# Kernel tuning notes

Hardware: AMD Instinct MI355X
Metric: run time of the kernel (lower is better)

## Reference

```python
import jax, jax.numpy as jnp
import numpy as np


def _segsum(x):
    """Stable segment sum: exp(segsum(A)) is 1-semiseparable. x: (..., T) -> (..., T, T)."""
    T = x.shape[-1]
    xx = jnp.broadcast_to(x[..., None], (*x.shape, T))
    xx = jnp.where(jnp.tril(jnp.ones((T, T), bool), -1), xx, 0.0)
    s = jnp.cumsum(xx, axis=-2)
    return jnp.where(jnp.tril(jnp.ones((T, T), bool), 0), s, -jnp.inf)


def setup_inputs() -> dict:
    key = jax.random.key(0)
    ks = jax.random.split(key, 6)
    b, T, h, p, n = 2, 1024, 32, 64, 128
    x = jax.random.normal(ks[0], (b, T, h, p), jnp.float32)
    # negative decay rates, as produced by -exp(A_log)*softplus(dt) in Mamba2
    A = -jax.random.uniform(ks[1], (b, T, h), jnp.float32, minval=0.01, maxval=0.5)
    B = jax.random.normal(ks[2], (b, T, h, n), jnp.float32)
    C = jax.random.normal(ks[3], (b, T, h, n), jnp.float32)
    # retrieval similarity mask (lower-triangular, like segment_and_cosine_similarity output)
    L_mask = jax.random.uniform(ks[4], (b, h, T, T), jnp.float32) * jnp.tril(jnp.ones((T, T), jnp.float32))
    mask_scaling_factor = jnp.float32(0.5)
    return {"x": x, "A": A, "B": B, "C": C, "L_mask": L_mask,
            "mask_scaling_factor": mask_scaling_factor, "chunk_size": 64}


def reference(x, A, B, C, L_mask, mask_scaling_factor, chunk_size):
    b, T, h, p = x.shape
    n = B.shape[-1]
    l = chunk_size
    k = T // l
    # chunk: b (c l) ... -> b c l ...
    xr = x.reshape(b, k, l, h, p)
    Br = B.reshape(b, k, l, h, n)
    Cr = C.reshape(b, k, l, h, n)
    Ar = jnp.transpose(A.reshape(b, k, l, h), (0, 3, 1, 2))  # b h c l
    A_cs = jnp.cumsum(Ar, axis=-1)                            # b h c l
    L = jnp.exp(_segsum(Ar))                                  # b h c l l
    # decompose_diagonal_and_lower_tri(L_mask, chunk_size)
    r = L_mask.reshape(b, h, k, l, k, l)
    didx = np.arange(k)
    L_mask_diag = jnp.moveaxis(r[:, :, didx, :, didx, :], 0, 2)          # b h k l l
    row_idx, col_idx = np.tril_indices(k, -1)                             # strict lower block pairs
    lower_tri = jnp.moveaxis(r[:, :, row_idx, :, col_idx, :], 0, 2)       # b h P l l
    L = L + mask_scaling_factor * L_mask_diag
    # diagonal (intra-chunk) blocks
    Y_diag = jnp.einsum('bclhn,bcshn,bhcls,bcshp->bclhp', Cr, Br, L, xr)
    # retrieval off-diagonal blocks, scatter-added back per destination chunk
    Y_tmp = jnp.einsum('bclhn,bcshn,bhcls,bcshp->bclhp',
                       Cr[:, row_idx], Br[:, col_idx],
                       mask_scaling_factor * lower_tri, xr[:, col_idx])   # b P l h p
    Y_retr = jnp.moveaxis(
        jax.ops.segment_sum(jnp.moveaxis(Y_tmp, 1, 0), jnp.asarray(row_idx), num_segments=k),
        0, 1)                                                             # b k l h p
    # inter-chunk state passing
    decay_states = jnp.exp(A_cs[..., -1:] - A_cs)                         # b h c l
    states = jnp.einsum('bclhn,bhcl,bclhp->bchpn', Br, decay_states, xr)  # b c h p n
    states = jnp.concatenate([jnp.zeros_like(states[:, :1]), states], axis=1)
    decay_chunk = jnp.exp(_segsum(jnp.pad(A_cs[..., -1], ((0, 0), (0, 0), (1, 0)))))  # b h (k+1) (k+1)
    new_states = jnp.einsum('bhzc,bchpn->bzhpn', decay_chunk, states)
    states_in, final_state = new_states[:, :-1], new_states[:, -1]
    Y_off = jnp.einsum('bclhn,bchpn,bhcl->bclhp', Cr, states_in, jnp.exp(A_cs))
    Y = (Y_diag + Y_off + Y_retr).reshape(b, T, h, p)
    return Y, final_state
```

## Files before the change

kernel.cpp:

```cpp
#include <hip/hip_runtime.h>

#define T_ 1024
#define H_ 32
#define P_ 64
#define N_ 128
#define L_ 64

typedef float f32x4 __attribute__((ext_vector_type(4)));
typedef short short8 __attribute__((ext_vector_type(8)));
typedef short short4v __attribute__((ext_vector_type(4)));
typedef unsigned int uint2v __attribute__((ext_vector_type(2)));
typedef unsigned int uint4v __attribute__((ext_vector_type(4)));

#define LOG2E 1.4426950408889634f

static __device__ __forceinline__ float bf2f(short s) {
  return __uint_as_float(((unsigned int)(unsigned short)s) << 16);
}

static __device__ __forceinline__ unsigned cvt_pk_bf16(float lo, float hi) {
  unsigned r;
  asm("v_cvt_pk_bf16_f32 %0, %1, %2" : "=v"(r) : "v"(lo), "v"(hi));
  return r;
}

static __device__ __forceinline__ float fexp2(float x) {
#if __has_builtin(__builtin_amdgcn_exp2f)
  return __builtin_amdgcn_exp2f(x);
#else
  return __expf(x * 0.6931471805599453f);
#endif
}

__global__ __launch_bounds__(256) void prep_kernel(
    const float* __restrict__ x, const float* __restrict__ Bm,
    const float* __restrict__ Cm, const float* __restrict__ A,
    short* __restrict__ Bbf, short* __restrict__ BT,
    short* __restrict__ Cbf, short* __restrict__ xT,
    float* __restrict__ cumA) {
  const int bh = blockIdx.x;
  const int tb = blockIdx.y;
  const int b = bh >> 5, h = bh & 31;
  const int tid = threadIdx.x;

  if (tb == 16) {
    __shared__ float sc[256];
    const int t0 = 4 * tid;
    const float a0 = A[(size_t)(b * T_ + t0 + 0) * H_ + h];
    const float a1 = A[(size_t)(b * T_ + t0 + 1) * H_ + h];
    const float a2 = A[(size_t)(b * T_ + t0 + 2) * H_ + h];
    const float a3 = A[(size_t)(b * T_ + t0 + 3) * H_ + h];
    const float p1 = a0 + a1, p2 = p1 + a2, p3 = p2 + a3;
    sc[tid] = p3;
    __syncthreads();
    for (int off = 1; off < 256; off <<= 1) {
      float v = (tid >= off) ? sc[tid - off] : 0.0f;
      __syncthreads();
      sc[tid] += v;
      __syncthreads();
    }
    const float base = sc[tid] - p3;
    float4 o;
    o.x = (base + a0) * LOG2E;
    o.y = (base + p1) * LOG2E;
    o.z = (base + p2) * LOG2E;
    o.w = (base + p3) * LOG2E;
    *(float4*)(cumA + (size_t)bh * T_ + t0) = o;
    return;
  }

  __shared__ short Bt[128][72];
  __shared__ short Xt[64][72];

#pragma unroll
  for (int i = 0; i < 8; ++i) {
    const int idx = tid + 256 * i;
    const int row = idx >> 5, n4 = idx & 31;
    const float4 v = *(const float4*)(Bm + ((size_t)(b * T_ + tb * 64 + row) * H_ + h) * N_ + n4 * 4);
    const unsigned p0 = cvt_pk_bf16(v.x, v.y);
    const unsigned p1 = cvt_pk_bf16(v.z, v.w);
    uint2v o; o.x = p0; o.y = p1;
    *(uint2v*)(Bbf + ((size_t)bh * T_ + tb * 64 + row) * N_ + n4 * 4) = o;
    Bt[n4 * 4 + 0][row] = (short)p0; Bt[n4 * 4 + 1][row] = (short)(p0 >> 16);
    Bt[n4 * 4 + 2][row] = (short)p1; Bt[n4 * 4 + 3][row] = (short)(p1 >> 16);
  }
#pragma unroll
  for (int i = 0; i < 8; ++i) {
    const int idx = tid + 256 * i;
    const int row = idx >> 5, n4 = idx & 31;
    const float4 v = *(const float4*)(Cm + ((size_t)(b * T_ + tb * 64 + row) * H_ + h) * N_ + n4 * 4);
    uint2v o; o.x = cvt_pk_bf16(v.x, v.y); o.y = cvt_pk_bf16(v.z, v.w);
    *(uint2v*)(Cbf + ((size_t)bh * T_ + tb * 64 + row) * N_ + n4 * 4) = o;
  }
#pragma unroll
  for (int i = 0; i < 4; ++i) {
    const int idx = tid + 256 * i;
    const int row = idx >> 4, p4 = idx & 15;
    const float4 v = *(const float4*)(x + ((size_t)(b * T_ + tb * 64 + row) * H_ + h) * P_ + p4 * 4);
    const unsigned p0 = cvt_pk_bf16(v.x, v.y);
    const unsigned p1 = cvt_pk_bf16(v.z, v.w);
    Xt[p4 * 4 + 0][row] = (short)p0;
    Xt[p4 * 4 + 1][row] = (short)(p0 >> 16);
    Xt[p4 * 4 + 2][row] = (short)p1;
    Xt[p4 * 4 + 3][row] = (short)(p1 >> 16);
  }
  __syncthreads();
#pragma unroll
  for (int i = 0; i < 4; ++i) {
    const int idx = tid + 256 * i;
    const int n = idx >> 3, t8 = idx & 7;
    const short4v a = *(const short4v*)&Bt[n][t8 * 8];
    const short4v c = *(const short4v*)&Bt[n][t8 * 8 + 4];
    short8 o;
    o[0] = a.x; o[1] = a.y; o[2] = a.z; o[3] = a.w;
    o[4] = c.x; o[5] = c.y; o[6] = c.z; o[7] = c.w;
    *(short8*)(BT + ((size_t)bh * N_ + n) * T_ + tb * 64 + t8 * 8) = o;
  }
#pragma unroll
  for (int i = 0; i < 2; ++i) {
    const int idx = tid + 256 * i;
    const int p = idx >> 3, t8 = idx & 7;
    const short4v a = *(const short4v*)&Xt[p][t8 * 8];
    const short4v c = *(const short4v*)&Xt[p][t8 * 8 + 4];
    short8 o;
    o[0] = a.x; o[1] = a.y; o[2] = a.z; o[3] = a.w;
    o[4] = c.x; o[5] = c.y; o[6] = c.z; o[7] = c.w;
    *(short8*)(xT + ((size_t)bh * P_ + p) * T_ + tb * 64 + t8 * 8) = o;
  }
}

__global__ __launch_bounds__(256, 2) void attn_kernel(
    const short* __restrict__ xT, const short* __restrict__ Bbf,
    const short* __restrict__ Cbf, const float* __restrict__ mask,
    const float* __restrict__ msf_p, const float* __restrict__ cumA,
    float* __restrict__ Y) {
  const int blk = blockIdx.x;
  const int bh = blk & 63;
  const int jj = blk >> 6;
  const int b = bh >> 5, h = bh & 31;
  const float msf = msf_p[0];
  const int tid = threadIdx.x;
  const int w = tid >> 6;
  const int lane = tid & 63;
  const int q = lane >> 4, c = lane & 15;

  __shared__ short Ps[4][16][72];

  const short* Bg0 = Bbf + (size_t)bh * T_ * N_ + 8 * q;
  const short* xg0 = xT + (size_t)bh * P_ * T_ + 8 * q;

#pragma unroll 1
  for (int pass = 0; pass < 2; ++pass) {
    const int qc = pass ? jj : (15 - jj);

    short8 cf[4];
    {
      const short* Cg = Cbf + ((size_t)bh * T_ + qc * L_ + 16 * w + c) * N_ + 8 * q;
#pragma unroll
      for (int kt = 0; kt < 4; ++kt) cf[kt] = *(const short8*)(Cg + kt * 32);
    }
    float ca_i[4];
#pragma unroll
    for (int r = 0; r < 4; ++r)
      ca_i[r] = cumA[bh * T_ + qc * L_ + 16 * w + 4 * q + r];

    f32x4 yacc[4];
#pragma unroll
    for (int pt = 0; pt < 4; ++pt) yacc[pt] = (f32x4){0.f, 0.f, 0.f, 0.f};

    const float* mrow0 = mask + ((size_t)bh * T_ + (size_t)(qc * L_ + 16 * w + 4 * q)) * T_ + c;

    float wgA[16], wgB[16];
    {
      float mv[16], ck[4];
#pragma unroll
      for (int tj = 0; tj < 4; ++tj)
#pragma unroll
        for (int r = 0; r < 4; ++r)
          mv[tj * 4 + r] = __builtin_nontemporal_load(mrow0 + (size_t)r * T_ + 16 * tj);
#pragma unroll
      for (int tj = 0; tj < 4; ++tj) ck[tj] = cumA[bh * T_ + 16 * tj + c];
#pragma unroll
      for (int tj = 0; tj < 4; ++tj)
#pragma unroll
        for (int r = 0; r < 4; ++r)
          wgA[tj * 4 + r] = fexp2(ca_i[r] - ck[tj]) + msf * mv[tj * 4 + r];
    }

#define ATTN_STEP(KC, WGI, WGO, DOPV)                                          \
  {                                                                            \
    const int kc_ = (KC);                                                      \
    const int kcn_ = (kc_ + 1 <= qc) ? (kc_ + 1) : qc;                         \
    short8 bfr[16];                                                            \
    const short* Bg = Bg0 + (size_t)kc_ * L_ * N_;                             \
    _Pragma("unroll") for (int kt = 0; kt < 4; ++kt)                           \
        _Pragma("unroll") for (int tj = 0; tj < 4; ++tj)                       \
            bfr[kt * 4 + tj] =                                                 \
        *(const short8*)(Bg + (size_t)(16 * tj + c) * N_ + kt * 32);           \
    short8 xfr[8];                                                             \
    if (DOPV) {                                                                \
      const short* xg = xg0 + (kc_ - 1) * L_;                                  \
      _Pragma("unroll") for (int kt2 = 0; kt2 < 2; ++kt2)                      \
          _Pragma("unroll") for (int pt = 0; pt < 4; ++pt)                     \
              xfr[kt2 * 4 + pt] =                                              \
          *(const short8*)(xg + (size_t)(16 * pt + c) * T_ + kt2 * 32);        \
    }                                                                          \
    float mv_[16], ck_[4];                                                     \
    const float* mb = mrow0 + (size_t)kcn_ * L_;                               \
    _Pragma("unroll") for (int tj = 0; tj < 4; ++tj)                           \
        _Pragma("unroll") for (int r = 0; r < 4; ++r)                          \
            mv_[tj * 4 + r] =                                                  \
        __builtin_nontemporal_load(mb + (size_t)r * T_ + 16 * tj);             \
    _Pragma("unroll") for (int tj = 0; tj < 4; ++tj)                           \
        ck_[tj] = cumA[bh * T_ + kcn_ * L_ + 16 * tj + c];                     \
    f32x4 sacc[4];                                                             \
    _Pragma("unroll") for (int tj = 0; tj < 4; ++tj)                           \
        sacc[tj] = (f32x4){0.f, 0.f, 0.f, 0.f};                                \
    __builtin_amdgcn_s_setprio(1);                                             \
    _Pragma("unroll") for (int kt = 0; kt < 4; ++kt)                           \
        _Pragma("unroll") for (int tj = 0; tj < 4; ++tj)                       \
            sacc[tj] = __builtin_amdgcn_mfma_f32_16x16x32_bf16(                \
        cf[kt], bfr[kt * 4 + tj], sacc[tj], 0, 0, 0);                          \
    __builtin_amdgcn_s_setprio(0);                                             \
    _Pragma("unroll") for (int tj = 0; tj < 4; ++tj)                           \
        _Pragma("unroll") for (int r = 0; r < 4; ++r)                          \
            WGO[tj * 4 + r] =                                                  \
        fexp2(ca_i[r] - ck_[tj]) + msf * mv_[tj * 4 + r];                      \
    const bool diag = (kc_ == qc);                                             \
    unsigned pw[8];                                                            \
    _Pragma("unroll") for (int tj = 0; tj < 4; ++tj) {                         \
      const int j_l = 16 * tj + c;                                             \
      float fv[4];                                                             \
      _Pragma("unroll") for (int r = 0; r < 4; ++r) {                          \
        const int i_l = 16 * w + 4 * q + r;                                    \
        fv[r] = (diag && j_l > i_l) ? 0.f : sacc[tj][r] * WGI[tj * 4 + r];     \
      }                                                                        \
      pw[tj * 2 + 0] = cvt_pk_bf16(fv[0], fv[1]);                              \
      pw[tj * 2 + 1] = cvt_pk_bf16(fv[2], fv[3]);                              \
    }                                                                          \
    if (DOPV) {                                                                \
      __builtin_amdgcn_s_setprio(1);                                           \
      _Pragma("unroll") for (int kt2 = 0; kt2 < 2; ++kt2) {                    \
        const short8 pf = *(const short8*)&Ps[w][c][kt2 * 32 + 8 * q];         \
        _Pragma("unroll") for (int pt = 0; pt < 4; ++pt)                       \
            yacc[pt] = __builtin_amdgcn_mfma_f32_16x16x32_bf16(                \
            pf, xfr[kt2 * 4 + pt], yacc[pt], 0, 0, 0);                         \
      }                                                                        \
      __builtin_amdgcn_s_setprio(0);                                           \
    }                                                                          \
    _Pragma("unroll") for (int tj = 0; tj < 4; ++tj) {                         \
      const int j_l = 16 * tj + c;                                             \
      Ps[w][4 * q + 0][j_l] = (short)pw[tj * 2 + 0];                           \
      Ps[w][4 * q + 1][j_l] = (short)(pw[tj * 2 + 0] >> 16);                   \
      Ps[w][4 * q + 2][j_l] = (short)pw[tj * 2 + 1];                           \
      Ps[w][4 * q + 3][j_l] = (short)(pw[tj * 2 + 1] >> 16);                   \
    }                                                                          \
  }

    ATTN_STEP(0, wgA, wgB, 0)
    int kc = 1;
    for (; kc + 1 <= qc; kc += 2) {
      ATTN_STEP(kc, wgB, wgA, 1)
      ATTN_STEP(kc + 1, wgA, wgB, 1)
    }
    if (kc <= qc) {
      ATTN_STEP(kc, wgB, wgA, 1)
    }
#undef ATTN_STEP

    {
      short8 xfr[8];
      const short* xg = xg0 + qc * L_;
#pragma unroll
      for (int kt2 = 0; kt2 < 2; ++kt2)
#pragma unroll
        for (int pt = 0; pt < 4; ++pt)
          xfr[kt2 * 4 + pt] = *(const short8*)(xg + (size_t)(16 * pt + c) * T_ + kt2 * 32);
      __builtin_amdgcn_s_setprio(1);
#pragma unroll
      for (int kt2 = 0; kt2 < 2; ++kt2) {
        const short8 pf = *(const short8*)&Ps[w][c][kt2 * 32 + 8 * q];
#pragma unroll
        for (int pt = 0; pt < 4; ++pt)
          yacc[pt] = __builtin_amdgcn_mfma_f32_16x16x32_bf16(
              pf, xfr[kt2 * 4 + pt], yacc[pt], 0, 0, 0);
      }
      __builtin_amdgcn_s_setprio(0);
    }

    float* Yg = Y + ((size_t)(b * T_ + qc * L_ + 16 * w + 4 * q) * H_ + h) * P_;
#pragma unroll
    for (int pt = 0; pt < 4; ++pt)
#pragma unroll
      for (int r = 0; r < 4; ++r)
        __builtin_nontemporal_store(yacc[pt][r], Yg + (size_t)r * (H_ * P_) + 16 * pt + c);
  }
}

__global__ __launch_bounds__(256) void state_kernel(
    const short* __restrict__ xT, const short* __restrict__ BT,
    const float* __restrict__ cumA, float* __restrict__ out) {
  const int bh = blockIdx.x;
  const int nh = blockIdx.y;
  const int tid = threadIdx.x;
  const int w = tid >> 6;
  const int lane = tid & 63;
  const int q = lane >> 4, c = lane & 15;

  __shared__ float wsh[1024];
  {
    const float cend = cumA[bh * T_ + (T_ - 1)];
    const float4 cv = *(const float4*)(cumA + (size_t)bh * T_ + 4 * tid);
    wsh[4 * tid + 0] = fexp2(cend - cv.x);
    wsh[4 * tid + 1] = fexp2(cend - cv.y);
    wsh[4 * tid + 2] = fexp2(cend - cv.z);
    wsh[4 * tid + 3] = fexp2(cend - cv.w);
  }
  __syncthreads();

  f32x4 acc[2];
#pragma unroll
  for (int nt = 0; nt < 2; ++nt) acc[nt] = (f32x4){0.f, 0.f, 0.f, 0.f};

#pragma unroll 4
  for (int ktl = 0; ktl < 32; ++ktl) {
    const int tg = ktl * 32;
    const short8 xv = *(const short8*)(xT + ((size_t)bh * P_ + 16 * w + c) * T_ + tg + 8 * q);
    const float4 w0 = *(const float4*)&wsh[tg + 8 * q];
    const float4 w1 = *(const float4*)&wsh[tg + 8 * q + 4];
    const float a0 = bf2f(xv[0]) * w0.x, a1 = bf2f(xv[1]) * w0.y;
    const float a2 = bf2f(xv[2]) * w0.z, a3 = bf2f(xv[3]) * w0.w;
    const float a4 = bf2f(xv[4]) * w1.x, a5 = bf2f(xv[5]) * w1.y;
    const float a6 = bf2f(xv[6]) * w1.z, a7 = bf2f(xv[7]) * w1.w;
    uint4v uu;
    uu.x = cvt_pk_bf16(a0, a1); uu.y = cvt_pk_bf16(a2, a3);
    uu.z = cvt_pk_bf16(a4, a5); uu.w = cvt_pk_bf16(a6, a7);
    const short8 af = __builtin_bit_cast(short8, uu);
#pragma unroll
    for (int nt = 0; nt < 2; ++nt) {
      const short8 bf = *(const short8*)(BT + ((size_t)bh * N_ + 32 * nh + 16 * nt + c) * T_ + tg + 8 * q);
      acc[nt] = __builtin_amdgcn_mfma_f32_16x16x32_bf16(af, bf, acc[nt], 0, 0, 0);
    }
  }

  float* o = out + (size_t)bh * P_ * N_;
#pragma unroll
  for (int nt = 0; nt < 2; ++nt)
#pragma unroll
    for (int r = 0; r < 4; ++r)
      __builtin_nontemporal_store(
          acc[nt][r], o + (size_t)(16 * w + 4 * q + r) * N_ + 32 * nh + 16 * nt + c);
}

extern "C" void kernel_launch(void* const* d_in, const int* in_sizes, int n_in,
                              void* d_out, int out_size, void* d_ws, size_t ws_size,
                              hipStream_t stream) {
  const float* x    = (const float*)d_in[0];
  const float* A    = (const float*)d_in[1];
  const float* Bm   = (const float*)d_in[2];
  const float* Cm   = (const float*)d_in[3];
  const float* mask = (const float*)d_in[4];
  const float* msf  = (const float*)d_in[5];
  float* Y  = (float*)d_out;
  float* fs = (float*)d_out + (size_t)2 * T_ * H_ * P_;

  char* ws = (char*)d_ws;
  float* cumA = (float*)ws;
  size_t off = 1 << 18;
  short* Bbf = (short*)(ws + off); off += (size_t)64 * T_ * N_ * 2;
  short* BT  = (short*)(ws + off); off += (size_t)64 * T_ * N_ * 2;
  short* Cbf = (short*)(ws + off); off += (size_t)64 * T_ * N_ * 2;
  short* xT  = (short*)(ws + off);

  prep_kernel<<<dim3(64, 17), 256, 0, stream>>>(x, Bm, Cm, A, Bbf, BT, Cbf, xT, cumA);
  attn_kernel<<<512, 256, 0, stream>>>(xT, Bbf, Cbf, mask, msf, cumA, Y);
  state_kernel<<<dim3(64, 4), 256, 0, stream>>>(xT, BT, cumA, fs);
}
```

Before: 491.5 us.

## Stream mask tiles into LDS with async global_load_lds double-buffering

Replaces the per-step nontemporal register loads of the retrieval mask with asynchronous global_load_lds copies into a double-buffered LDS tile, prefetched two chunks ahead. Each step then reads its mask values from LDS. The per-block cumA row is staged once in LDS so the repeated global reads of it go away. The aim is to hide mask-load latency behind the MFMA work and cut vector register pressure. In exchange it adds about 36KB of LDS per block, which may cap occupancy at the 2 blocks per CU the launch bounds ask for. It also depends on hand-written vmcnt waits that must match the exact count of outstanding loads.

```diff
diff --git a/kernel.cpp b/kernel.cpp
--- a/kernel.cpp
+++ b/kernel.cpp
@@ -30,6 +30,12 @@
 #else
   return __expf(x * 0.6931471805599453f);
 #endif
+}
+
+static __device__ __forceinline__ void gload_lds16(const float* g, float* l) {
+  __builtin_amdgcn_global_load_lds(
+      (const __attribute__((address_space(1))) void*)g,
+      (__attribute__((address_space(3))) void*)l, 16, 0, 0);
 }
 
 __global__ __launch_bounds__(256) void prep_kernel(
@@ -145,6 +151,21 @@
   const int q = lane >> 4, c = lane & 15;
 
   __shared__ short Ps[4][16][72];
+  __shared__ float Msk[2][4][1024];
+  __shared__ float CA[1024];
+
+  {
+    const float4 cv = *(const float4*)(cumA + (size_t)bh * T_ + 4 * tid);
+    *(float4*)&CA[4 * tid] = cv;
+  }
+  __syncthreads();
+
+  int moff[4], mt[4];
+#pragma unroll
+  for (int j = 0; j < 4; ++j) {
+    moff[j] = (4 * j + (lane >> 4)) * T_ + ((4 * (lane & 15) + 16 * j) & 63);
+    mt[j] = q * 256 + c + 16 * ((j - q) & 3);
+  }
 
   const short* Bg0 = Bbf + (size_t)bh * T_ * N_ + 8 * q;
   const short* xg0 = xT + (size_t)bh * P_ * T_ + 8 * q;
@@ -153,6 +174,16 @@
   for (int pass = 0; pass < 2; ++pass) {
     const int qc = pass ? jj : (15 - jj);
 
+    const float* tbase0 = mask + ((size_t)bh * T_ + (size_t)(qc * L_ + 16 * w)) * T_;
+
+    {
+      const int t1 = (1 <= qc) ? 1 : qc;
+      const float* g = tbase0 + (size_t)t1 * L_;
+#pragma unroll
+      for (int j = 0; j < 4; ++j)
+        gload_lds16(g + moff[j], &Msk[1][w][j * 256]);
+    }
+
     short8 cf[4];
     {
       const short* Cg = Cbf + ((size_t)bh * T_ + qc * L_ + 16 * w + c) * N_ + 8 * q;
@@ -161,8 +192,7 @@
     }
     float ca_i[4];
 #pragma unroll
-    for (int r = 0; r < 4; ++r)
-      ca_i[r] = cumA[bh * T_ + qc * L_ + 16 * w + 4 * q + r];
+    for (int r = 0; r < 4; ++r) ca_i[r] = CA[qc * 64 + 16 * w + 4 * q + r];
 
     f32x4 yacc[4];
 #pragma unroll
@@ -172,25 +202,26 @@
 
     float wgA[16], wgB[16];
     {
-      float mv[16], ck[4];
+      float mv[16];
 #pragma unroll
       for (int tj = 0; tj < 4; ++tj)
 #pragma unroll
         for (int r = 0; r < 4; ++r)
           mv[tj * 4 + r] = __builtin_nontemporal_load(mrow0 + (size_t)r * T_ + 16 * tj);
 #pragma unroll
-      for (int tj = 0; tj < 4; ++tj) ck[tj] = cumA[bh * T_ + 16 * tj + c];
-#pragma unroll
-      for (int tj = 0; tj < 4; ++tj)
+      for (int tj = 0; tj < 4; ++tj) {
+        const float ck = CA[16 * tj + c];
 #pragma unroll
         for (int r = 0; r < 4; ++r)
-          wgA[tj * 4 + r] = fexp2(ca_i[r] - ck[tj]) + msf * mv[tj * 4 + r];
-    }
-
-#define ATTN_STEP(KC, WGI, WGO, DOPV)                                          \
+          wgA[tj * 4 + r] = fexp2(ca_i[r] - ck) + msf * mv[tj * 4 + r];
+      }
+    }
+
+#define ATTN_STEP(KC, WGI, WGO, WB, RB, DOPV)                                  \
   {                                                                            \
     const int kc_ = (KC);                                                      \
     const int kcn_ = (kc_ + 1 <= qc) ? (kc_ + 1) : qc;                         \
+    const int kc2_ = (kc_ + 2 <= qc) ? (kc_ + 2) : qc;                         \
     short8 bfr[16];                                                            \
     const short* Bg = Bg0 + (size_t)kc_ * L_ * N_;                             \
     _Pragma("unroll") for (int kt = 0; kt < 4; ++kt)                           \
@@ -205,14 +236,11 @@
               xfr[kt2 * 4 + pt] =                                              \
           *(const short8*)(xg + (size_t)(16 * pt + c) * T_ + kt2 * 32);        \
     }                                                                          \
-    float mv_[16], ck_[4];                                                     \
-    const float* mb = mrow0 + (size_t)kcn_ * L_;                               \
-    _Pragma("unroll") for (int tj = 0; tj < 4; ++tj)                           \
-        _Pragma("unroll") for (int r = 0; r < 4; ++r)                          \
-            mv_[tj * 4 + r] =                                                  \
-        __builtin_nontemporal_load(mb + (size_t)r * T_ + 16 * tj);             \
-    _Pragma("unroll") for (int tj = 0; tj < 4; ++tj)                           \
-        ck_[tj] = cumA[bh * T_ + kcn_ * L_ + 16 * tj + c];                     \
+    {                                                                          \
+      const float* mg = tbase0 + (size_t)kc2_ * L_;                            \
+      _Pragma("unroll") for (int j = 0; j < 4; ++j)                            \
+          gload_lds16(mg + moff[j], &Msk[WB][w][j * 256]);                     \
+    }                                                                          \
     f32x4 sacc[4];                                                             \
     _Pragma("unroll") for (int tj = 0; tj < 4; ++tj)                           \
         sacc[tj] = (f32x4){0.f, 0.f, 0.f, 0.f};                                \
@@ -222,10 +250,17 @@
             sacc[tj] = __builtin_amdgcn_mfma_f32_16x16x32_bf16(                \
         cf[kt], bfr[kt * 4 + tj], sacc[tj], 0, 0, 0);                          \
     __builtin_amdgcn_s_setprio(0);                                             \
-    _Pragma("unroll") for (int tj = 0; tj < 4; ++tj)                           \
-        _Pragma("unroll") for (int r = 0; r < 4; ++r)                          \
-            WGO[tj * 4 + r] =                                                  \
-        fexp2(ca_i[r] - ck_[tj]) + msf * mv_[tj * 4 + r];                      \
+    if (DOPV) {                                                                \
+      asm volatile("s_waitcnt vmcnt(12)" ::: "memory");                        \
+    } else {                                                                   \
+      asm volatile("s_waitcnt vmcnt(4)" ::: "memory");                         \
+    }                                                                          \
+    _Pragma("unroll") for (int tj = 0; tj < 4; ++tj) {                         \
+      const float ck = CA[kcn_ * 64 + 16 * tj + c];                            \
+      _Pragma("unroll") for (int r = 0; r < 4; ++r)                            \
+          WGO[tj * 4 + r] =                                                    \
+          fexp2(ca_i[r] - ck) + msf * Msk[RB][w][mt[tj] + r * 64];             \
+    }                                                                          \
     const bool diag = (kc_ == qc);                                             \
     unsigned pw[8];                                                            \
     _Pragma("unroll") for (int tj = 0; tj < 4; ++tj) {                         \
@@ -257,14 +292,14 @@
     }                                                                          \
   }
 
-    ATTN_STEP(0, wgA, wgB, 0)
+    ATTN_STEP(0, wgA, wgB, 0, 1, 0)
     int kc = 1;
     for (; kc + 1 <= qc; kc += 2) {
-      ATTN_STEP(kc, wgB, wgA, 1)
-      ATTN_STEP(kc + 1, wgA, wgB, 1)
+      ATTN_STEP(kc, wgB, wgA, 1, 0, 1)
+      ATTN_STEP(kc + 1, wgA, wgB, 0, 1, 1)
     }
     if (kc <= qc) {
-      ATTN_STEP(kc, wgB, wgA, 1)
+      ATTN_STEP(kc, wgB, wgA, 1, 0, 1)
     }
 #undef ATTN_STEP
 
```

After: 490.7 us. About the same (-0.2%).
